# Kernel optimization log

Measured on AMD Instinct MI355X. Metric: run time of the kernel, lower is better.

Reference implementation:

```python
import jax, jax.numpy as jnp
import numpy as np

H, DK, DV = 16, 64, 64
DECAY = 0.99
WRITE_STRENGTH = 1.0


def setup_inputs() -> dict:
    key = jax.random.key(0)
    ks = jax.random.split(key, 7)
    B, S, D = 4, 4096, 2048
    sd = 1.0 / np.sqrt(D)
    return {
        "hidden": jax.random.normal(ks[0], (B, S, D), jnp.float32),
        "memory": jax.random.normal(ks[1], (H, DK, DV), jnp.float32) * 0.02,
        "Wk": jax.random.normal(ks[2], (H * DK, D), jnp.float32) * sd,
        "Wv": jax.random.normal(ks[3], (H * DV, D), jnp.float32) * sd,
        "Wq": jax.random.normal(ks[4], (H * DK, D), jnp.float32) * sd,
        "Wg": jax.random.normal(ks[5], (D, D), jnp.float32) * sd,
        "Wo": jax.random.normal(ks[6], (D, H * DV), jnp.float32) * (1.0 / np.sqrt(H * DV)),
    }


def reference(hidden, memory, Wk, Wv, Wq, Wg, Wo):
    B, S, D = hidden.shape
    # projections (Linear, bias=False): x @ W^T
    k = (hidden @ Wk.T).reshape(B, S, H, DK)
    v = (hidden @ Wv.T).reshape(B, S, H, DV)
    q = (hidden @ Wq.T).reshape(B, S, H, DK)
    # read with pre-update memory: r = q^T M
    readout = jnp.einsum('bshk,hkv->bshv', q, memory).reshape(B, S, H * DV)
    # output gate: h' = h + sigmoid(Wg h) * (Wo r)
    gate = jax.nn.sigmoid(hidden @ Wg.T)
    out = hidden + gate * (readout @ Wo.T)
    # decaying outer-product write: M' = lambda*M + rho * sum_i k_i v_i^T
    new_memory = DECAY * memory + WRITE_STRENGTH * jnp.einsum('bshk,bshv->hkv', k, v)
    return out, new_memory
```

## Files before the change

### kernel.cpp

```cpp
#include <hip/hip_runtime.h>
#include <hip/hip_bf16.h>

typedef __attribute__((ext_vector_type(4))) float f32x4;
typedef __bf16 bf16x8 __attribute__((ext_vector_type(8)));
typedef int int4v __attribute__((ext_vector_type(4)));

#define TOKENS 16384
#define DIM    2048
#define NKVQ   3072

__device__ __forceinline__ void gload_lds16(const void* g, void* l) {
  __builtin_amdgcn_global_load_lds((const __attribute__((address_space(1))) void*)g,
                                   (__attribute__((address_space(3))) void*)l, 16, 0, 0);
}

__global__ void cast8_kernel(const float* __restrict__ src, __bf16* __restrict__ dst, int n8) {
  int i = blockIdx.x * blockDim.x + threadIdx.x;
  if (i >= n8) return;
  const float4* s = (const float4*)src;
  float4 a = s[2 * i], b = s[2 * i + 1];
  bf16x8 o;
  o[0] = (__bf16)a.x; o[1] = (__bf16)a.y; o[2] = (__bf16)a.z; o[3] = (__bf16)a.w;
  o[4] = (__bf16)b.x; o[5] = (__bf16)b.y; o[6] = (__bf16)b.z; o[7] = (__bf16)b.w;
  ((bf16x8*)dst)[i] = o;
}

__global__ void weff_kernel(const float* __restrict__ Wo, const float* __restrict__ mem,
                            __bf16* __restrict__ Weff) {
  int idx = blockIdx.x * blockDim.x + threadIdx.x;
  int d = idx >> 10, hk = idx & 1023, h = hk >> 6;
  const float* wo = Wo + d * 1024 + h * 64;
  const float* mm = mem + hk * 64;
  float s = 0.f;
  #pragma unroll 8
  for (int v = 0; v < 64; ++v) s += wo[v] * mm[v];
  Weff[idx] = (__bf16)s;
}

__device__ __forceinline__ void gemm256_core(
    const __bf16* __restrict__ A, int lda,
    const __bf16* __restrict__ B, int ldb,
    int m0, int n0, int nt, char* sm, f32x4 acc[8][4]) {

  const int tid = threadIdx.x, lane = tid & 63, wid = tid >> 6;
  const int wr = wid >> 2, wc = wid & 3;
  const int lrow = lane & 15, kc = lane >> 4;

  int offA[8], offB[4];
  #pragma unroll
  for (int m = 0; m < 8; ++m) {
    int u = (wr * 128 + m * 16 + lrow) * 4 + kc;
    offA[m] = (u ^ ((u >> 3) & 7)) << 4;
  }
  #pragma unroll
  for (int n = 0; n < 4; ++n) {
    int u = (wc * 64 + n * 16 + lrow) * 4 + kc;
    offB[n] = ((u ^ ((u >> 3) & 7)) << 4) + 16384;
  }

  const __bf16* pSA[2]; const __bf16* pSB[2];
  #pragma unroll
  for (int s = 0; s < 2; ++s) {
    int U = s * 512 + tid;
    int u = U ^ ((U >> 3) & 7);
    pSA[s] = A + (size_t)(m0 + (u >> 2)) * lda + (u & 3) * 8;
    pSB[s] = B + (size_t)(n0 + (u >> 2)) * ldb + (u & 3) * 8;
  }

  bf16x8 bvS0[4], bvS1[4];

#define BARX() asm volatile("s_barrier" ::: "memory")
#define VM4()  asm volatile("s_waitcnt vmcnt(4)" ::: "memory")
#define VM0()  asm volatile("s_waitcnt vmcnt(0)" ::: "memory")
#define NOVM
#define NOSTAGE
#define STAGE(bb, tt) do { \
    char* sA = sm + (bb) * 32768 + tid * 16; \
    gload_lds16(pSA[0] + (tt) * 32, sA); \
    gload_lds16(pSA[1] + (tt) * 32, sA + 8192); \
    gload_lds16(pSB[0] + (tt) * 32, sA + 16384); \
    gload_lds16(pSB[1] + (tt) * 32, sA + 24576); } while (0)

#define PH(bufC, bufN, C, N, STG, WT) do { \
    const char* bC = sm + (bufC) * 32768; \
    const char* bN = sm + (bufN) * 32768; \
    bf16x8 av[8]; \
    _Pragma("unroll") for (int m = 0; m < 8; ++m) av[m] = *(const bf16x8*)(bC + offA[m]); \
    _Pragma("unroll") for (int n = 0; n < 4; ++n) bvS##N[n] = *(const bf16x8*)(bN + offB[n]); \
    STG; \
    __builtin_amdgcn_s_setprio(1); \
    _Pragma("unroll") for (int m = 0; m < 8; ++m) \
      _Pragma("unroll") for (int n = 0; n < 4; ++n) \
        acc[m][n] = __builtin_amdgcn_mfma_f32_16x16x32_bf16(av[m], bvS##C[n], acc[m][n], 0, 0, 0); \
    __builtin_amdgcn_s_setprio(0); \
    WT; BARX(); } while (0)

#define PHF(bufC, C) do { \
    const char* bC = sm + (bufC) * 32768; \
    bf16x8 av[8]; \
    _Pragma("unroll") for (int m = 0; m < 8; ++m) av[m] = *(const bf16x8*)(bC + offA[m]); \
    __builtin_amdgcn_s_setprio(1); \
    _Pragma("unroll") for (int m = 0; m < 8; ++m) \
      _Pragma("unroll") for (int n = 0; n < 4; ++n) \
        acc[m][n] = __builtin_amdgcn_mfma_f32_16x16x32_bf16(av[m], bvS##C[n], acc[m][n], 0, 0, 0); \
    __builtin_amdgcn_s_setprio(0); } while (0)

  STAGE(0, 0); STAGE(1, 1); STAGE(2, 2);
  VM4(); BARX();
  #pragma unroll
  for (int n = 0; n < 4; ++n) bvS0[n] = *(const bf16x8*)(sm + offB[n]);

  for (int i = 0, e = (nt - 4) >> 2; i < e; ++i) {
    const int t = i << 2;
    PH(0, 1, 0, 1, STAGE(3, t + 3), VM4());
    PH(1, 2, 1, 0, STAGE(0, t + 4), VM4());
    PH(2, 3, 0, 1, STAGE(1, t + 5), VM4());
    PH(3, 0, 1, 0, STAGE(2, t + 6), VM4());
  }
  PH(0, 1, 0, 1, STAGE(3, nt - 1), VM4());
  PH(1, 2, 1, 0, NOSTAGE, VM0());
  PH(2, 3, 0, 1, NOSTAGE, NOVM);
  PHF(3, 1);
#undef PH
#undef PHF
#undef STAGE
#undef BARX
#undef VM4
#undef VM0
#undef NOVM
#undef NOSTAGE
}

__global__ void __launch_bounds__(512, 1)
gemm_fused_kernel(const __bf16* __restrict__ Xb, const __bf16* __restrict__ W1,
                  __bf16* __restrict__ Y, __bf16* __restrict__ Gb) {
  __shared__ __attribute__((aligned(16))) char smem[131072];
  const int x = blockIdx.x & 7;
  const int l = blockIdx.x >> 3;
  const int bm = x * 8 + (l & 7);
  const int bn = l >> 3;
  const int m0 = bm * 256, n0 = bn * 256;
  f32x4 acc[8][4] = {};
  gemm256_core(Xb, DIM, W1, DIM, m0, n0, 64, smem, acc);

  __syncthreads();
  const int tid = threadIdx.x, wid = tid >> 6, lane = tid & 63;
  const int wr = wid >> 2, wc = wid & 3;
  const int crow = (lane >> 4) << 2, ccol = lane & 15;
  const bool isY = bn < 12;
  #pragma unroll
  for (int f = 0; f < 8; ++f)
    #pragma unroll
    for (int n = 0; n < 4; ++n)
      #pragma unroll
      for (int j = 0; j < 4; ++j) {
        int r = wr * 128 + f * 16 + crow + j;
        int c = wc * 64 + n * 16 + ccol;
        float v = acc[f][n][j];
        if (!isY) v = 1.0f / (1.0f + __expf(-v));
        *(__bf16*)(smem + r * 512 + ((c * 2) ^ ((r & 7) << 4))) = (__bf16)v;
      }
  __syncthreads();
  const int rsub = tid >> 5, ch = tid & 31;
  if (isY) {
    #pragma unroll
    for (int p = 0; p < 16; ++p) {
      int r = p * 16 + rsub;
      bf16x8 v = *(const bf16x8*)(smem + r * 512 + ((ch * 16) ^ ((r & 7) << 4)));
      __builtin_nontemporal_store(__builtin_bit_cast(int4v, v),
          (int4v*)(Y + (size_t)(m0 + r) * NKVQ + n0 + ch * 8));
    }
  } else {
    const int c0 = n0 - 3072;
    #pragma unroll
    for (int p = 0; p < 16; ++p) {
      int r = p * 16 + rsub;
      bf16x8 v = *(const bf16x8*)(smem + r * 512 + ((ch * 16) ^ ((r & 7) << 4)));
      __builtin_nontemporal_store(__builtin_bit_cast(int4v, v),
          (int4v*)(Gb + (size_t)(m0 + r) * DIM + c0 + ch * 8));
    }
  }
}

__global__ void __launch_bounds__(512, 1)
gemm_read_kernel(const __bf16* __restrict__ Yq, const __bf16* __restrict__ Weff,
                 const __bf16* __restrict__ Gb, const float* __restrict__ hidden,
                 float* __restrict__ out) {
  __shared__ __attribute__((aligned(16))) char smem[131072];
  const int x = blockIdx.x & 7;
  const int l = blockIdx.x >> 3;
  const int bm = x * 8 + (l & 7);
  const int bn = l >> 3;
  const int m0 = bm * 256, n0 = bn * 256;
  f32x4 acc[8][4] = {};
  gemm256_core(Yq, NKVQ, Weff, 1024, m0, n0, 32, smem, acc);

  const int tid = threadIdx.x, wid = tid >> 6, lane = tid & 63;
  const int wr = wid >> 2, wc = wid & 3;
  const int crow = (lane >> 4) << 2, ccol = lane & 15;
  #pragma unroll
  for (int f = 0; f < 8; ++f) {
    int row = m0 + wr * 128 + f * 16 + crow;
    #pragma unroll
    for (int n = 0; n < 4; ++n) {
      int col = n0 + wc * 64 + n * 16 + ccol;
      #pragma unroll
      for (int j = 0; j < 4; ++j) {
        size_t idx = (size_t)(row + j) * DIM + col;
        out[idx] = hidden[idx] + (float)Gb[idx] * acc[f][n][j];
      }
    }
  }
}

__global__ void __launch_bounds__(256)
mem_update_kernel(const __bf16* __restrict__ Y, float* __restrict__ part) {
  const int h = blockIdx.x & 15, sp = blockIdx.x >> 4;
  __shared__ __attribute__((aligned(16))) __bf16 KT[64 * 32];
  __shared__ __attribute__((aligned(16))) __bf16 VT[64 * 32];
  const int tid = threadIdx.x, wid = tid >> 6, lane = tid & 63;
  const int lrow = lane & 15, lk = (lane >> 4) * 8;
  const __bf16* Kbase = Y + (size_t)sp * 1024 * NKVQ + h * 64;
  const __bf16* Vbase = Kbase + 1024;
  f32x4 acc[4] = {};
  const int t = tid >> 3, c8 = (tid & 7) * 8;
  for (int t0 = 0; t0 < 1024; t0 += 32) {
    __syncthreads();
    bf16x8 kv = *(const bf16x8*)(Kbase + (size_t)(t0 + t) * NKVQ + c8);
    bf16x8 vv = *(const bf16x8*)(Vbase + (size_t)(t0 + t) * NKVQ + c8);
    #pragma unroll
    for (int j = 0; j < 8; ++j) {
      KT[(c8 + j) * 32 + t] = kv[j];
      VT[(c8 + j) * 32 + t] = vv[j];
    }
    __syncthreads();
    bf16x8 af = *(const bf16x8*)(KT + (wid * 16 + lrow) * 32 + lk);
    #pragma unroll
    for (int n = 0; n < 4; ++n) {
      bf16x8 bf_ = *(const bf16x8*)(VT + (n * 16 + lrow) * 32 + lk);
      acc[n] = __builtin_amdgcn_mfma_f32_16x16x32_bf16(af, bf_, acc[n], 0, 0, 0);
    }
  }
  float* pp = part + ((size_t)sp * 16 + h) * 4096;
  const int crow = wid * 16 + (lane >> 4) * 4, ccol = lane & 15;
  #pragma unroll
  for (int n = 0; n < 4; ++n)
    #pragma unroll
    for (int r = 0; r < 4; ++r)
      pp[(crow + r) * 64 + n * 16 + ccol] = acc[n][r];
}

__global__ void mem_reduce_kernel(const float* __restrict__ part, const float* __restrict__ mem,
                                  float* __restrict__ out) {
  int i = blockIdx.x * blockDim.x + threadIdx.x;
  float s = 0.99f * mem[i];
  #pragma unroll
  for (int sp = 0; sp < 16; ++sp) s += part[sp * 65536 + i];
  out[i] = s;
}

extern "C" void kernel_launch(void* const* d_in, const int* in_sizes, int n_in,
                              void* d_out, int out_size, void* d_ws, size_t ws_size,
                              hipStream_t stream) {
  const float* hidden = (const float*)d_in[0];
  const float* memory = (const float*)d_in[1];
  const float* Wk = (const float*)d_in[2];
  const float* Wv = (const float*)d_in[3];
  const float* Wq = (const float*)d_in[4];
  const float* Wg = (const float*)d_in[5];
  const float* Wo = (const float*)d_in[6];
  float* out = (float*)d_out;
  float* mem_out = out + (size_t)TOKENS * DIM;

  char* ws = (char*)d_ws;
  __bf16* Xb   = (__bf16*)(ws);
  __bf16* W1   = (__bf16*)(ws + 67108864);
  __bf16* Weff = (__bf16*)(ws + 88080384);
  __bf16* Yb   = (__bf16*)(ws + 92274688);
  __bf16* Gb   = (__bf16*)(ws + 192937984);
  float*  part = (float*)(ws + 260046848);

  cast8_kernel<<<16384, 256, 0, stream>>>(hidden, Xb, 4194304);
  cast8_kernel<<<1024, 256, 0, stream>>>(Wk, W1, 262144);
  cast8_kernel<<<1024, 256, 0, stream>>>(Wv, W1 + 2097152, 262144);
  cast8_kernel<<<1024, 256, 0, stream>>>(Wq, W1 + 4194304, 262144);
  cast8_kernel<<<2048, 256, 0, stream>>>(Wg, W1 + 6291456, 524288);
  weff_kernel<<<8192, 256, 0, stream>>>(Wo, memory, Weff);

  gemm_fused_kernel<<<1280, 512, 0, stream>>>(Xb, W1, Yb, Gb);
  gemm_read_kernel<<<512, 512, 0, stream>>>(Yb + 2048, Weff, Gb, hidden, out);

  mem_update_kernel<<<256, 256, 0, stream>>>(Yb, part);
  mem_reduce_kernel<<<256, 256, 0, stream>>>(part, memory, mem_out);
}
```

Measured before the change: 630.2 us.

## Use 4 waves with 128x128 per-wave tiles and double-buffered register fragments

Result: slower. 700.3 us (+11.1%).

```diff
diff --git a/kernel.cpp b/kernel.cpp
--- a/kernel.cpp
+++ b/kernel.cpp
@@ -40,98 +40,100 @@
 __device__ __forceinline__ void gemm256_core(
     const __bf16* __restrict__ A, int lda,
     const __bf16* __restrict__ B, int ldb,
-    int m0, int n0, int nt, char* sm, f32x4 acc[8][4]) {
+    int m0, int n0, int nt, char* sm, f32x4 acc[8][8]) {
 
   const int tid = threadIdx.x, lane = tid & 63, wid = tid >> 6;
-  const int wr = wid >> 2, wc = wid & 3;
+  const int wr = wid >> 1, wc = wid & 1;
   const int lrow = lane & 15, kc = lane >> 4;
 
-  int offA[8], offB[4];
+  int offA[8], offB[8];
   #pragma unroll
   for (int m = 0; m < 8; ++m) {
     int u = (wr * 128 + m * 16 + lrow) * 4 + kc;
     offA[m] = (u ^ ((u >> 3) & 7)) << 4;
   }
   #pragma unroll
-  for (int n = 0; n < 4; ++n) {
-    int u = (wc * 64 + n * 16 + lrow) * 4 + kc;
+  for (int n = 0; n < 8; ++n) {
+    int u = (wc * 128 + n * 16 + lrow) * 4 + kc;
     offB[n] = ((u ^ ((u >> 3) & 7)) << 4) + 16384;
   }
 
-  const __bf16* pSA[2]; const __bf16* pSB[2];
-  #pragma unroll
-  for (int s = 0; s < 2; ++s) {
-    int U = s * 512 + tid;
+  const __bf16* pSA[4]; const __bf16* pSB[4];
+  #pragma unroll
+  for (int s = 0; s < 4; ++s) {
+    int U = s * 256 + tid;
     int u = U ^ ((U >> 3) & 7);
     pSA[s] = A + (size_t)(m0 + (u >> 2)) * lda + (u & 3) * 8;
     pSB[s] = B + (size_t)(n0 + (u >> 2)) * ldb + (u & 3) * 8;
   }
 
-  bf16x8 bvS0[4], bvS1[4];
+  bf16x8 avSA[8], avSB[8], bvSA[8], bvSB[8];
 
 #define BARX() asm volatile("s_barrier" ::: "memory")
-#define VM4()  asm volatile("s_waitcnt vmcnt(4)" ::: "memory")
+#define VM8()  asm volatile("s_waitcnt vmcnt(8)" ::: "memory")
 #define VM0()  asm volatile("s_waitcnt vmcnt(0)" ::: "memory")
 #define NOVM
 #define NOSTAGE
 #define STAGE(bb, tt) do { \
     char* sA = sm + (bb) * 32768 + tid * 16; \
     gload_lds16(pSA[0] + (tt) * 32, sA); \
-    gload_lds16(pSA[1] + (tt) * 32, sA + 8192); \
+    gload_lds16(pSA[1] + (tt) * 32, sA + 4096); \
+    gload_lds16(pSA[2] + (tt) * 32, sA + 8192); \
+    gload_lds16(pSA[3] + (tt) * 32, sA + 12288); \
     gload_lds16(pSB[0] + (tt) * 32, sA + 16384); \
-    gload_lds16(pSB[1] + (tt) * 32, sA + 24576); } while (0)
-
-#define PH(bufC, bufN, C, N, STG, WT) do { \
-    const char* bC = sm + (bufC) * 32768; \
+    gload_lds16(pSB[1] + (tt) * 32, sA + 20480); \
+    gload_lds16(pSB[2] + (tt) * 32, sA + 24576); \
+    gload_lds16(pSB[3] + (tt) * 32, sA + 28672); } while (0)
+
+#define PH(bufN, C, N, STG, WT) do { \
     const char* bN = sm + (bufN) * 32768; \
-    bf16x8 av[8]; \
-    _Pragma("unroll") for (int m = 0; m < 8; ++m) av[m] = *(const bf16x8*)(bC + offA[m]); \
-    _Pragma("unroll") for (int n = 0; n < 4; ++n) bvS##N[n] = *(const bf16x8*)(bN + offB[n]); \
+    _Pragma("unroll") for (int m = 0; m < 8; ++m) avS##N[m] = *(const bf16x8*)(bN + offA[m]); \
+    _Pragma("unroll") for (int n = 0; n < 8; ++n) bvS##N[n] = *(const bf16x8*)(bN + offB[n]); \
     STG; \
+    __builtin_amdgcn_sched_barrier(0); \
     __builtin_amdgcn_s_setprio(1); \
     _Pragma("unroll") for (int m = 0; m < 8; ++m) \
-      _Pragma("unroll") for (int n = 0; n < 4; ++n) \
-        acc[m][n] = __builtin_amdgcn_mfma_f32_16x16x32_bf16(av[m], bvS##C[n], acc[m][n], 0, 0, 0); \
+      _Pragma("unroll") for (int n = 0; n < 8; ++n) \
+        acc[m][n] = __builtin_amdgcn_mfma_f32_16x16x32_bf16(avS##C[m], bvS##C[n], acc[m][n], 0, 0, 0); \
     __builtin_amdgcn_s_setprio(0); \
     WT; BARX(); } while (0)
 
-#define PHF(bufC, C) do { \
-    const char* bC = sm + (bufC) * 32768; \
-    bf16x8 av[8]; \
-    _Pragma("unroll") for (int m = 0; m < 8; ++m) av[m] = *(const bf16x8*)(bC + offA[m]); \
+#define PHF(C) do { \
     __builtin_amdgcn_s_setprio(1); \
     _Pragma("unroll") for (int m = 0; m < 8; ++m) \
-      _Pragma("unroll") for (int n = 0; n < 4; ++n) \
-        acc[m][n] = __builtin_amdgcn_mfma_f32_16x16x32_bf16(av[m], bvS##C[n], acc[m][n], 0, 0, 0); \
+      _Pragma("unroll") for (int n = 0; n < 8; ++n) \
+        acc[m][n] = __builtin_amdgcn_mfma_f32_16x16x32_bf16(avS##C[m], bvS##C[n], acc[m][n], 0, 0, 0); \
     __builtin_amdgcn_s_setprio(0); } while (0)
 
   STAGE(0, 0); STAGE(1, 1); STAGE(2, 2);
-  VM4(); BARX();
-  #pragma unroll
-  for (int n = 0; n < 4; ++n) bvS0[n] = *(const bf16x8*)(sm + offB[n]);
+  VM8(); BARX();
+  #pragma unroll
+  for (int m = 0; m < 8; ++m) avSA[m] = *(const bf16x8*)(sm + offA[m]);
+  #pragma unroll
+  for (int n = 0; n < 8; ++n) bvSA[n] = *(const bf16x8*)(sm + offB[n]);
 
   for (int i = 0, e = (nt - 4) >> 2; i < e; ++i) {
     const int t = i << 2;
-    PH(0, 1, 0, 1, STAGE(3, t + 3), VM4());
-    PH(1, 2, 1, 0, STAGE(0, t + 4), VM4());
-    PH(2, 3, 0, 1, STAGE(1, t + 5), VM4());
-    PH(3, 0, 1, 0, STAGE(2, t + 6), VM4());
-  }
-  PH(0, 1, 0, 1, STAGE(3, nt - 1), VM4());
-  PH(1, 2, 1, 0, NOSTAGE, VM0());
-  PH(2, 3, 0, 1, NOSTAGE, NOVM);
-  PHF(3, 1);
+    PH(1, A, B, STAGE(3, t + 3), VM8());
+    PH(2, B, A, STAGE(0, t + 4), VM8());
+    PH(3, A, B, STAGE(1, t + 5), VM8());
+    PH(0, B, A, STAGE(2, t + 6), VM8());
+  }
+  PH(1, A, B, STAGE(3, nt - 1), VM8());
+  PH(2, B, A, NOSTAGE, VM0());
+  PH(3, A, B, NOSTAGE, NOVM);
+  PHF(B);
 #undef PH
 #undef PHF
 #undef STAGE
 #undef BARX
-#undef VM4
+#undef VM8
 #undef VM0
 #undef NOVM
 #undef NOSTAGE
 }
 
-__global__ void __launch_bounds__(512, 1)
+__global__ void __launch_bounds__(256, 1)
 gemm_fused_kernel(const __bf16* __restrict__ Xb, const __bf16* __restrict__ W1,
                   __bf16* __restrict__ Y, __bf16* __restrict__ Gb) {
   __shared__ __attribute__((aligned(16))) char smem[131072];
@@ -140,22 +142,22 @@
   const int bm = x * 8 + (l & 7);
   const int bn = l >> 3;
   const int m0 = bm * 256, n0 = bn * 256;
-  f32x4 acc[8][4] = {};
+  f32x4 acc[8][8] = {};
   gemm256_core(Xb, DIM, W1, DIM, m0, n0, 64, smem, acc);
 
   __syncthreads();
   const int tid = threadIdx.x, wid = tid >> 6, lane = tid & 63;
-  const int wr = wid >> 2, wc = wid & 3;
+  const int wr = wid >> 1, wc = wid & 1;
   const int crow = (lane >> 4) << 2, ccol = lane & 15;
   const bool isY = bn < 12;
   #pragma unroll
   for (int f = 0; f < 8; ++f)
     #pragma unroll
-    for (int n = 0; n < 4; ++n)
+    for (int n = 0; n < 8; ++n)
       #pragma unroll
       for (int j = 0; j < 4; ++j) {
         int r = wr * 128 + f * 16 + crow + j;
-        int c = wc * 64 + n * 16 + ccol;
+        int c = wc * 128 + n * 16 + ccol;
         float v = acc[f][n][j];
         if (!isY) v = 1.0f / (1.0f + __expf(-v));
         *(__bf16*)(smem + r * 512 + ((c * 2) ^ ((r & 7) << 4))) = (__bf16)v;
@@ -164,8 +166,8 @@
   const int rsub = tid >> 5, ch = tid & 31;
   if (isY) {
     #pragma unroll
-    for (int p = 0; p < 16; ++p) {
-      int r = p * 16 + rsub;
+    for (int p = 0; p < 32; ++p) {
+      int r = p * 8 + rsub;
       bf16x8 v = *(const bf16x8*)(smem + r * 512 + ((ch * 16) ^ ((r & 7) << 4)));
       __builtin_nontemporal_store(__builtin_bit_cast(int4v, v),
           (int4v*)(Y + (size_t)(m0 + r) * NKVQ + n0 + ch * 8));
@@ -173,8 +175,8 @@
   } else {
     const int c0 = n0 - 3072;
     #pragma unroll
-    for (int p = 0; p < 16; ++p) {
-      int r = p * 16 + rsub;
+    for (int p = 0; p < 32; ++p) {
+      int r = p * 8 + rsub;
       bf16x8 v = *(const bf16x8*)(smem + r * 512 + ((ch * 16) ^ ((r & 7) << 4)));
       __builtin_nontemporal_store(__builtin_bit_cast(int4v, v),
           (int4v*)(Gb + (size_t)(m0 + r) * DIM + c0 + ch * 8));
@@ -182,7 +184,7 @@
   }
 }
 
-__global__ void __launch_bounds__(512, 1)
+__global__ void __launch_bounds__(256, 1)
 gemm_read_kernel(const __bf16* __restrict__ Yq, const __bf16* __restrict__ Weff,
                  const __bf16* __restrict__ Gb, const float* __restrict__ hidden,
                  float* __restrict__ out) {
@@ -192,18 +194,18 @@
   const int bm = x * 8 + (l & 7);
   const int bn = l >> 3;
   const int m0 = bm * 256, n0 = bn * 256;
-  f32x4 acc[8][4] = {};
+  f32x4 acc[8][8] = {};
   gemm256_core(Yq, NKVQ, Weff, 1024, m0, n0, 32, smem, acc);
 
   const int tid = threadIdx.x, wid = tid >> 6, lane = tid & 63;
-  const int wr = wid >> 2, wc = wid & 3;
+  const int wr = wid >> 1, wc = wid & 1;
   const int crow = (lane >> 4) << 2, ccol = lane & 15;
   #pragma unroll
   for (int f = 0; f < 8; ++f) {
     int row = m0 + wr * 128 + f * 16 + crow;
     #pragma unroll
-    for (int n = 0; n < 4; ++n) {
-      int col = n0 + wc * 64 + n * 16 + ccol;
+    for (int n = 0; n < 8; ++n) {
+      int col = n0 + wc * 128 + n * 16 + ccol;
       #pragma unroll
       for (int j = 0; j < 4; ++j) {
         size_t idx = (size_t)(row + j) * DIM + col;
@@ -287,8 +289,8 @@
   cast8_kernel<<<2048, 256, 0, stream>>>(Wg, W1 + 6291456, 524288);
   weff_kernel<<<8192, 256, 0, stream>>>(Wo, memory, Weff);
 
-  gemm_fused_kernel<<<1280, 512, 0, stream>>>(Xb, W1, Yb, Gb);
-  gemm_read_kernel<<<512, 512, 0, stream>>>(Yb + 2048, Weff, Gb, hidden, out);
+  gemm_fused_kernel<<<1280, 256, 0, stream>>>(Xb, W1, Yb, Gb);
+  gemm_read_kernel<<<512, 256, 0, stream>>>(Yb + 2048, Weff, Gb, hidden, out);
 
   mem_update_kernel<<<256, 256, 0, stream>>>(Yb, part);
   mem_reduce_kernel<<<256, 256, 0, stream>>>(part, memory, mem_out);
```

## Restructure GEMM core to K=64 tiles with double-buffered quadrant-phased pipeline

Applied to the files above, without the earlier changes.

Result: faster. 605.9 us (-3.9%).

```diff
diff --git a/kernel.cpp b/kernel.cpp
--- a/kernel.cpp
+++ b/kernel.cpp
@@ -44,91 +44,108 @@
 
   const int tid = threadIdx.x, lane = tid & 63, wid = tid >> 6;
   const int wr = wid >> 2, wc = wid & 3;
-  const int lrow = lane & 15, kc = lane >> 4;
-
-  int offA[8], offB[4];
-  #pragma unroll
-  for (int m = 0; m < 8; ++m) {
-    int u = (wr * 128 + m * 16 + lrow) * 4 + kc;
-    offA[m] = (u ^ ((u >> 3) & 7)) << 4;
+  const int lrow = lane & 15, kc = lane >> 4, s7 = lrow & 7;
+
+  const int rowA = (wr * 64 + lrow) * 128;
+  const int rowB = (wc * 32 + lrow) * 128 + 32768;
+  const int sw0 = ((0 + kc) ^ s7) << 4;
+  const int sw1 = ((4 + kc) ^ s7) << 4;
+
+  unsigned oa[2][2], ob[2][2];
+  #pragma unroll
+  for (int h = 0; h < 2; ++h)
+    #pragma unroll
+    for (int L = 0; L < 2; ++L) {
+      int l = h * 1024 + L * 512 + tid;
+      int rl = l >> 3;
+      int c  = (l & 7) ^ (rl & 7);
+      int ra = ((rl & 127) >> 6) * 128 + h * 64 + (rl & 63);
+      int rb = ((rl & 127) >> 5) * 64  + h * 32 + (rl & 31);
+      oa[h][L] = (unsigned)(((m0 + ra) * lda + c * 8) * 2);
+      ob[h][L] = (unsigned)(((n0 + rb) * ldb + c * 8) * 2);
+    }
+  const char* Ab = (const char*)A;
+  const char* Bb = (const char*)B;
+
+  bf16x8 avA[4][2], avB[4][2], bvA[2][2], bvB[2][2];
+
+#define BARX() asm volatile("s_barrier" ::: "memory")
+#define VM2()  asm volatile("s_waitcnt vmcnt(2)" ::: "memory")
+#define VM0()  asm volatile("s_waitcnt vmcnt(0)" ::: "memory")
+#define STA(bb, h, tt) do { \
+    gload_lds16(Ab + oa[h][0] + (tt) * 128, sm + (bb) * 65536 + ((h) * 1024 + tid) * 16); \
+    gload_lds16(Ab + oa[h][1] + (tt) * 128, sm + (bb) * 65536 + ((h) * 1024 + 512 + tid) * 16); } while (0)
+#define STB(bb, h, tt) do { \
+    gload_lds16(Bb + ob[h][0] + (tt) * 128, sm + (bb) * 65536 + 32768 + ((h) * 1024 + tid) * 16); \
+    gload_lds16(Bb + ob[h][1] + (tt) * 128, sm + (bb) * 65536 + 32768 + ((h) * 1024 + 512 + tid) * 16); } while (0)
+#define RD_AV(dst, bb, mh) \
+    _Pragma("unroll") for (int f = 0; f < 4; ++f) { \
+      dst[f][0] = *(const bf16x8*)(sm + (bb) * 65536 + (mh) * 16384 + rowA + f * 2048 + sw0); \
+      dst[f][1] = *(const bf16x8*)(sm + (bb) * 65536 + (mh) * 16384 + rowA + f * 2048 + sw1); }
+#define RD_BV(dst, bb, nh) \
+    _Pragma("unroll") for (int n = 0; n < 2; ++n) { \
+      dst[n][0] = *(const bf16x8*)(sm + (bb) * 65536 + (nh) * 16384 + rowB + n * 2048 + sw0); \
+      dst[n][1] = *(const bf16x8*)(sm + (bb) * 65536 + (nh) * 16384 + rowB + n * 2048 + sw1); }
+#define MM(av, bv, fo, no) do { \
+    __builtin_amdgcn_s_setprio(1); \
+    _Pragma("unroll") for (int f = 0; f < 4; ++f) \
+      _Pragma("unroll") for (int n = 0; n < 2; ++n) { \
+        acc[(fo) + f][(no) + n] = __builtin_amdgcn_mfma_f32_16x16x32_bf16(av[f][0], bv[n][0], acc[(fo) + f][(no) + n], 0, 0, 0); \
+        acc[(fo) + f][(no) + n] = __builtin_amdgcn_mfma_f32_16x16x32_bf16(av[f][1], bv[n][1], acc[(fo) + f][(no) + n], 0, 0, 0); } \
+    __builtin_amdgcn_s_setprio(0); } while (0)
+
+#define TILE_PH(c, d, t) do { \
+    RD_AV(avA, c, 0); RD_BV(bvA, c, 0); \
+    STA(d, 0, (t) + 1); \
+    BARX(); \
+    MM(avA, bvA, 0, 0); \
+    VM2(); BARX(); \
+    RD_BV(bvB, c, 1); \
+    STA(d, 1, (t) + 1); \
+    BARX(); \
+    MM(avA, bvB, 0, 2); \
+    BARX(); \
+    RD_AV(avB, c, 1); \
+    STB(d, 0, (t) + 1); \
+    BARX(); \
+    MM(avB, bvB, 4, 2); \
+    BARX(); \
+    STB(d, 1, (t) + 1); \
+    BARX(); \
+    MM(avB, bvA, 4, 0); \
+    VM2(); BARX(); } while (0)
+
+#define TILE_TAIL(c) do { \
+    RD_AV(avA, c, 0); RD_BV(bvA, c, 0); \
+    BARX(); \
+    MM(avA, bvA, 0, 0); \
+    VM0(); \
+    RD_BV(bvB, c, 1); \
+    MM(avA, bvB, 0, 2); \
+    RD_AV(avB, c, 1); \
+    MM(avB, bvB, 4, 2); \
+    MM(avB, bvA, 4, 0); } while (0)
+
+  STA(0, 0, 0); STA(0, 1, 0); STB(0, 0, 0); STB(0, 1, 0);
+  VM2(); BARX();
+
+  for (int i = 0, e = (nt - 2) >> 1; i < e; ++i) {
+    const int t = i << 1;
+    TILE_PH(0, 1, t);
+    TILE_PH(1, 0, t + 1);
   }
-  #pragma unroll
-  for (int n = 0; n < 4; ++n) {
-    int u = (wc * 64 + n * 16 + lrow) * 4 + kc;
-    offB[n] = ((u ^ ((u >> 3) & 7)) << 4) + 16384;
-  }
-
-  const __bf16* pSA[2]; const __bf16* pSB[2];
-  #pragma unroll
-  for (int s = 0; s < 2; ++s) {
-    int U = s * 512 + tid;
-    int u = U ^ ((U >> 3) & 7);
-    pSA[s] = A + (size_t)(m0 + (u >> 2)) * lda + (u & 3) * 8;
-    pSB[s] = B + (size_t)(n0 + (u >> 2)) * ldb + (u & 3) * 8;
-  }
-
-  bf16x8 bvS0[4], bvS1[4];
-
-#define BARX() asm volatile("s_barrier" ::: "memory")
-#define VM4()  asm volatile("s_waitcnt vmcnt(4)" ::: "memory")
-#define VM0()  asm volatile("s_waitcnt vmcnt(0)" ::: "memory")
-#define NOVM
-#define NOSTAGE
-#define STAGE(bb, tt) do { \
-    char* sA = sm + (bb) * 32768 + tid * 16; \
-    gload_lds16(pSA[0] + (tt) * 32, sA); \
-    gload_lds16(pSA[1] + (tt) * 32, sA + 8192); \
-    gload_lds16(pSB[0] + (tt) * 32, sA + 16384); \
-    gload_lds16(pSB[1] + (tt) * 32, sA + 24576); } while (0)
-
-#define PH(bufC, bufN, C, N, STG, WT) do { \
-    const char* bC = sm + (bufC) * 32768; \
-    const char* bN = sm + (bufN) * 32768; \
-    bf16x8 av[8]; \
-    _Pragma("unroll") for (int m = 0; m < 8; ++m) av[m] = *(const bf16x8*)(bC + offA[m]); \
-    _Pragma("unroll") for (int n = 0; n < 4; ++n) bvS##N[n] = *(const bf16x8*)(bN + offB[n]); \
-    STG; \
-    __builtin_amdgcn_s_setprio(1); \
-    _Pragma("unroll") for (int m = 0; m < 8; ++m) \
-      _Pragma("unroll") for (int n = 0; n < 4; ++n) \
-        acc[m][n] = __builtin_amdgcn_mfma_f32_16x16x32_bf16(av[m], bvS##C[n], acc[m][n], 0, 0, 0); \
-    __builtin_amdgcn_s_setprio(0); \
-    WT; BARX(); } while (0)
-
-#define PHF(bufC, C) do { \
-    const char* bC = sm + (bufC) * 32768; \
-    bf16x8 av[8]; \
-    _Pragma("unroll") for (int m = 0; m < 8; ++m) av[m] = *(const bf16x8*)(bC + offA[m]); \
-    __builtin_amdgcn_s_setprio(1); \
-    _Pragma("unroll") for (int m = 0; m < 8; ++m) \
-      _Pragma("unroll") for (int n = 0; n < 4; ++n) \
-        acc[m][n] = __builtin_amdgcn_mfma_f32_16x16x32_bf16(av[m], bvS##C[n], acc[m][n], 0, 0, 0); \
-    __builtin_amdgcn_s_setprio(0); } while (0)
-
-  STAGE(0, 0); STAGE(1, 1); STAGE(2, 2);
-  VM4(); BARX();
-  #pragma unroll
-  for (int n = 0; n < 4; ++n) bvS0[n] = *(const bf16x8*)(sm + offB[n]);
-
-  for (int i = 0, e = (nt - 4) >> 2; i < e; ++i) {
-    const int t = i << 2;
-    PH(0, 1, 0, 1, STAGE(3, t + 3), VM4());
-    PH(1, 2, 1, 0, STAGE(0, t + 4), VM4());
-    PH(2, 3, 0, 1, STAGE(1, t + 5), VM4());
-    PH(3, 0, 1, 0, STAGE(2, t + 6), VM4());
-  }
-  PH(0, 1, 0, 1, STAGE(3, nt - 1), VM4());
-  PH(1, 2, 1, 0, NOSTAGE, VM0());
-  PH(2, 3, 0, 1, NOSTAGE, NOVM);
-  PHF(3, 1);
-#undef PH
-#undef PHF
-#undef STAGE
+  TILE_PH(0, 1, nt - 2);
+  TILE_TAIL(1);
+#undef TILE_PH
+#undef TILE_TAIL
+#undef MM
+#undef RD_AV
+#undef RD_BV
+#undef STA
+#undef STB
 #undef BARX
-#undef VM4
+#undef VM2
 #undef VM0
-#undef NOVM
-#undef NOSTAGE
 }
 
 __global__ void __launch_bounds__(512, 1)
@@ -141,7 +158,7 @@
   const int bn = l >> 3;
   const int m0 = bm * 256, n0 = bn * 256;
   f32x4 acc[8][4] = {};
-  gemm256_core(Xb, DIM, W1, DIM, m0, n0, 64, smem, acc);
+  gemm256_core(Xb, DIM, W1, DIM, m0, n0, 32, smem, acc);
 
   __syncthreads();
   const int tid = threadIdx.x, wid = tid >> 6, lane = tid & 63;
@@ -193,7 +210,7 @@
   const int bn = l >> 3;
   const int m0 = bm * 256, n0 = bn * 256;
   f32x4 acc[8][4] = {};
-  gemm256_core(Yq, NKVQ, Weff, 1024, m0, n0, 32, smem, acc);
+  gemm256_core(Yq, NKVQ, Weff, 1024, m0, n0, 16, smem, acc);
 
   const int tid = threadIdx.x, wid = tid >> 6, lane = tid & 63;
   const int wr = wid >> 2, wc = wid & 3;
```

## Fold Wq into Wo·M weight product and fuse gate+readout into one GEMM

Applied to the files above, without the earlier changes.

Measured after the change: 597.5 us. 5.2% less time.

```diff
diff --git a/kernel.cpp b/kernel.cpp
--- a/kernel.cpp
+++ b/kernel.cpp
@@ -3,6 +3,7 @@
 
 typedef __attribute__((ext_vector_type(4))) float f32x4;
 typedef __bf16 bf16x8 __attribute__((ext_vector_type(8)));
+typedef __bf16 bf16x4 __attribute__((ext_vector_type(4)));
 typedef int int4v __attribute__((ext_vector_type(4)));
 
 #define TOKENS 16384
@@ -23,6 +24,42 @@
   o[0] = (__bf16)a.x; o[1] = (__bf16)a.y; o[2] = (__bf16)a.z; o[3] = (__bf16)a.w;
   o[4] = (__bf16)b.x; o[5] = (__bf16)b.y; o[6] = (__bf16)b.z; o[7] = (__bf16)b.w;
   ((bf16x8*)dst)[i] = o;
+}
+
+__global__ void castWg_inter_kernel(const float* __restrict__ Wg, __bf16* __restrict__ W1) {
+  int i = blockIdx.x * blockDim.x + threadIdx.x;
+  int g = i >> 8, c8 = (i & 255) * 8;
+  const float4* s = (const float4*)(Wg + (size_t)g * DIM + c8);
+  float4 a = s[0], b = s[1];
+  bf16x8 o;
+  o[0] = (__bf16)a.x; o[1] = (__bf16)a.y; o[2] = (__bf16)a.z; o[3] = (__bf16)a.w;
+  o[4] = (__bf16)b.x; o[5] = (__bf16)b.y; o[6] = (__bf16)b.z; o[7] = (__bf16)b.w;
+  int r = 32 * (g >> 4) + (g & 15);
+  *(bf16x8*)(W1 + (size_t)r * DIM + c8) = o;
+}
+
+__global__ void __launch_bounds__(256)
+transWq_kernel(const float* __restrict__ Wq, __bf16* __restrict__ WqT) {
+  __shared__ __bf16 Ts[64][68];
+  const int ti = blockIdx.x >> 5, di = blockIdx.x & 31;
+  const int h0 = ti << 6, d0 = di << 6;
+  const int t = threadIdx.x, r0 = t >> 4, c4 = t & 15;
+  #pragma unroll
+  for (int i = 0; i < 4; ++i) {
+    int row = r0 + i * 16;
+    float4 v = *(const float4*)(Wq + (size_t)(h0 + row) * DIM + d0 + c4 * 4);
+    Ts[row][c4 * 4 + 0] = (__bf16)v.x; Ts[row][c4 * 4 + 1] = (__bf16)v.y;
+    Ts[row][c4 * 4 + 2] = (__bf16)v.z; Ts[row][c4 * 4 + 3] = (__bf16)v.w;
+  }
+  __syncthreads();
+  const int d = t >> 2, sq = t & 3;
+  #pragma unroll
+  for (int g = 0; g < 2; ++g) {
+    bf16x8 o;
+    #pragma unroll
+    for (int k = 0; k < 8; ++k) o[k] = Ts[sq * 16 + g * 8 + k][d];
+    *(bf16x8*)(WqT + (size_t)(d0 + d) * 1024 + h0 + sq * 16 + g * 8) = o;
+  }
 }
 
 __global__ void weff_kernel(const float* __restrict__ Wo, const float* __restrict__ mem,
@@ -132,8 +169,35 @@
 }
 
 __global__ void __launch_bounds__(512, 1)
-gemm_fused_kernel(const __bf16* __restrict__ Xb, const __bf16* __restrict__ W1,
-                  __bf16* __restrict__ Y, __bf16* __restrict__ Gb) {
+w2_kernel(const __bf16* __restrict__ Weff, const __bf16* __restrict__ WqT,
+          __bf16* __restrict__ W1) {
+  __shared__ __attribute__((aligned(16))) char smem[131072];
+  const int bm = blockIdx.x >> 3, bn = blockIdx.x & 7;
+  const int m0 = bm * 256, n0 = bn * 256;
+  f32x4 acc[8][4] = {};
+  gemm256_core(Weff, 1024, WqT, 1024, m0, n0, 32, smem, acc);
+
+  const int tid = threadIdx.x, wid = tid >> 6, lane = tid & 63;
+  const int wr = wid >> 2, wc = wid & 3;
+  const int crow = (lane >> 4) << 2, ccol = lane & 15;
+  #pragma unroll
+  for (int f = 0; f < 8; ++f) {
+    int base16 = (m0 + wr * 128) >> 4;
+    #pragma unroll
+    for (int n = 0; n < 4; ++n) {
+      int col = n0 + wc * 64 + n * 16 + ccol;
+      #pragma unroll
+      for (int j = 0; j < 4; ++j) {
+        int r = 32 * (base16 + f) + 16 + crow + j;
+        W1[(size_t)r * DIM + col] = (__bf16)acc[f][n][j];
+      }
+    }
+  }
+}
+
+__global__ void __launch_bounds__(512, 1)
+gemm_main_kernel(const __bf16* __restrict__ Xb, const __bf16* __restrict__ W1,
+                 const float* __restrict__ hidden, float* __restrict__ out) {
   __shared__ __attribute__((aligned(16))) char smem[131072];
   const int x = blockIdx.x & 7;
   const int l = blockIdx.x >> 3;
@@ -143,49 +207,28 @@
   f32x4 acc[8][4] = {};
   gemm256_core(Xb, DIM, W1, DIM, m0, n0, 64, smem, acc);
 
-  __syncthreads();
   const int tid = threadIdx.x, wid = tid >> 6, lane = tid & 63;
   const int wr = wid >> 2, wc = wid & 3;
   const int crow = (lane >> 4) << 2, ccol = lane & 15;
-  const bool isY = bn < 12;
-  #pragma unroll
-  for (int f = 0; f < 8; ++f)
-    #pragma unroll
-    for (int n = 0; n < 4; ++n)
+  #pragma unroll
+  for (int f = 0; f < 8; ++f) {
+    int row = m0 + wr * 128 + f * 16 + crow;
+    #pragma unroll
+    for (int np = 0; np < 2; ++np) {
+      int col = (n0 >> 1) + wc * 32 + np * 16 + ccol;
       #pragma unroll
       for (int j = 0; j < 4; ++j) {
-        int r = wr * 128 + f * 16 + crow + j;
-        int c = wc * 64 + n * 16 + ccol;
-        float v = acc[f][n][j];
-        if (!isY) v = 1.0f / (1.0f + __expf(-v));
-        *(__bf16*)(smem + r * 512 + ((c * 2) ^ ((r & 7) << 4))) = (__bf16)v;
+        size_t idx = (size_t)(row + j) * DIM + col;
+        float gv = 1.0f / (1.0f + __expf(-acc[f][2 * np][j]));
+        out[idx] = hidden[idx] + gv * acc[f][2 * np + 1][j];
       }
-  __syncthreads();
-  const int rsub = tid >> 5, ch = tid & 31;
-  if (isY) {
-    #pragma unroll
-    for (int p = 0; p < 16; ++p) {
-      int r = p * 16 + rsub;
-      bf16x8 v = *(const bf16x8*)(smem + r * 512 + ((ch * 16) ^ ((r & 7) << 4)));
-      __builtin_nontemporal_store(__builtin_bit_cast(int4v, v),
-          (int4v*)(Y + (size_t)(m0 + r) * NKVQ + n0 + ch * 8));
     }
-  } else {
-    const int c0 = n0 - 3072;
-    #pragma unroll
-    for (int p = 0; p < 16; ++p) {
-      int r = p * 16 + rsub;
-      bf16x8 v = *(const bf16x8*)(smem + r * 512 + ((ch * 16) ^ ((r & 7) << 4)));
-      __builtin_nontemporal_store(__builtin_bit_cast(int4v, v),
-          (int4v*)(Gb + (size_t)(m0 + r) * DIM + c0 + ch * 8));
-    }
   }
 }
 
 __global__ void __launch_bounds__(512, 1)
-gemm_read_kernel(const __bf16* __restrict__ Yq, const __bf16* __restrict__ Weff,
-                 const __bf16* __restrict__ Gb, const float* __restrict__ hidden,
-                 float* __restrict__ out) {
+gemm_kv_kernel(const __bf16* __restrict__ Xb, const __bf16* __restrict__ Wkv,
+               __bf16* __restrict__ Yb) {
   __shared__ __attribute__((aligned(16))) char smem[131072];
   const int x = blockIdx.x & 7;
   const int l = blockIdx.x >> 3;
@@ -193,23 +236,30 @@
   const int bn = l >> 3;
   const int m0 = bm * 256, n0 = bn * 256;
   f32x4 acc[8][4] = {};
-  gemm256_core(Yq, NKVQ, Weff, 1024, m0, n0, 32, smem, acc);
-
+  gemm256_core(Xb, DIM, Wkv, DIM, m0, n0, 64, smem, acc);
+
+  __syncthreads();
   const int tid = threadIdx.x, wid = tid >> 6, lane = tid & 63;
   const int wr = wid >> 2, wc = wid & 3;
   const int crow = (lane >> 4) << 2, ccol = lane & 15;
   #pragma unroll
-  for (int f = 0; f < 8; ++f) {
-    int row = m0 + wr * 128 + f * 16 + crow;
-    #pragma unroll
-    for (int n = 0; n < 4; ++n) {
-      int col = n0 + wc * 64 + n * 16 + ccol;
+  for (int f = 0; f < 8; ++f)
+    #pragma unroll
+    for (int n = 0; n < 4; ++n)
       #pragma unroll
       for (int j = 0; j < 4; ++j) {
-        size_t idx = (size_t)(row + j) * DIM + col;
-        out[idx] = hidden[idx] + (float)Gb[idx] * acc[f][n][j];
+        int r = wr * 128 + f * 16 + crow + j;
+        int c = wc * 64 + n * 16 + ccol;
+        *(__bf16*)(smem + r * 512 + ((c * 2) ^ ((r & 7) << 4))) = (__bf16)acc[f][n][j];
       }
-    }
+  __syncthreads();
+  const int rsub = tid >> 5, ch = tid & 31;
+  #pragma unroll
+  for (int p = 0; p < 16; ++p) {
+    int r = p * 16 + rsub;
+    bf16x8 v = *(const bf16x8*)(smem + r * 512 + ((ch * 16) ^ ((r & 7) << 4)));
+    __builtin_nontemporal_store(__builtin_bit_cast(int4v, v),
+        (int4v*)(Yb + (size_t)(m0 + r) * NKVQ + n0 + ch * 8));
   }
 }
 
@@ -275,20 +325,23 @@
   char* ws = (char*)d_ws;
   __bf16* Xb   = (__bf16*)(ws);
   __bf16* W1   = (__bf16*)(ws + 67108864);
-  __bf16* Weff = (__bf16*)(ws + 88080384);
-  __bf16* Yb   = (__bf16*)(ws + 92274688);
-  __bf16* Gb   = (__bf16*)(ws + 192937984);
-  float*  part = (float*)(ws + 260046848);
+  __bf16* Wkv  = (__bf16*)(ws + 83886080);
+  __bf16* Weff = (__bf16*)(ws + 92274688);
+  __bf16* WqT  = (__bf16*)(ws + 96468992);
+  __bf16* Yb   = (__bf16*)(ws + 100663296);
+  float*  part = (float*)(ws + 201326592);
 
   cast8_kernel<<<16384, 256, 0, stream>>>(hidden, Xb, 4194304);
-  cast8_kernel<<<1024, 256, 0, stream>>>(Wk, W1, 262144);
-  cast8_kernel<<<1024, 256, 0, stream>>>(Wv, W1 + 2097152, 262144);
-  cast8_kernel<<<1024, 256, 0, stream>>>(Wq, W1 + 4194304, 262144);
-  cast8_kernel<<<2048, 256, 0, stream>>>(Wg, W1 + 6291456, 524288);
+  castWg_inter_kernel<<<2048, 256, 0, stream>>>(Wg, W1);
+  cast8_kernel<<<1024, 256, 0, stream>>>(Wk, Wkv, 262144);
+  cast8_kernel<<<1024, 256, 0, stream>>>(Wv, Wkv + 2097152, 262144);
   weff_kernel<<<8192, 256, 0, stream>>>(Wo, memory, Weff);
-
-  gemm_fused_kernel<<<1280, 512, 0, stream>>>(Xb, W1, Yb, Gb);
-  gemm_read_kernel<<<512, 512, 0, stream>>>(Yb + 2048, Weff, Gb, hidden, out);
+  transWq_kernel<<<512, 256, 0, stream>>>(Wq, WqT);
+
+  w2_kernel<<<64, 512, 0, stream>>>(Weff, WqT, W1);
+
+  gemm_main_kernel<<<1024, 512, 0, stream>>>(Xb, W1, hidden, out);
+  gemm_kv_kernel<<<512, 512, 0, stream>>>(Xb, Wkv, Yb);
 
   mem_update_kernel<<<256, 256, 0, stream>>>(Yb, part);
   mem_reduce_kernel<<<256, 256, 0, stream>>>(part, memory, mem_out);
```
